# Performance work log

Measured on AMD Instinct MI355X. Metric: run time of the kernel, lower is better.

## Reference

```python
import jax, jax.numpy as jnp
import numpy as np

B, L, HID, NH = 8, 384, 512, 8
DH = HID // NH
MAX_SEQ_LEN = 384  # module's max_seq_len; pe has 2*MAX_SEQ_LEN rows


def setup_inputs() -> dict:
    key = jax.random.key(0)
    ks = jax.random.split(key, 16)
    s = 0.02
    inp = {
        "key": jax.random.normal(ks[0], (B, L, HID), jnp.float32),
        "query": jax.random.normal(ks[1], (B, L, HID), jnp.float32),
        "value": jax.random.normal(ks[2], (B, L, HID), jnp.float32),
        "seq_len": jnp.maximum(
            jax.random.randint(ks[3], (B,), L // 2, L + 1), 0
        ).at[0].set(L),  # ensure max(seq_len) == L
        "pe": jax.random.normal(ks[4], (2 * MAX_SEQ_LEN, HID), jnp.float32) * s,
        "Wk": jax.random.normal(ks[5], (HID, HID), jnp.float32) * s,
        "bk": jnp.zeros((HID,), jnp.float32),
        "Wq": jax.random.normal(ks[6], (HID, HID), jnp.float32) * s,
        "bq": jnp.zeros((HID,), jnp.float32),
        "Wv": jax.random.normal(ks[7], (HID, HID), jnp.float32) * s,
        "bv": jnp.zeros((HID,), jnp.float32),
        "Wr": jax.random.normal(ks[8], (HID, HID), jnp.float32) * s,
        "br": jnp.zeros((HID,), jnp.float32),
        "u_bias": jax.random.normal(ks[9], (NH, DH), jnp.float32) * s,
        "v_bias": jax.random.normal(ks[10], (NH, DH), jnp.float32) * s,
        "Wf": jax.random.normal(ks[11], (HID, HID), jnp.float32) * s,
        "bf": jnp.zeros((HID,), jnp.float32),
    }
    return inp


def reference(key, query, value, seq_len, pe, Wk, bk, Wq, bq, Wv, bv, Wr, br,
              u_bias, v_bias, Wf, bf):
    b, l, hid = key.shape
    # relative distance matrix: rel[i, j] = j - i
    idx = jnp.arange(l)
    rel = idx[None, :] - idx[:, None]                       # [L, L]
    rpe = pe[rel + MAX_SEQ_LEN]                             # [L, L, HID] gather

    k = (key @ Wk.T + bk).reshape(b, l, NH, DH).transpose(0, 2, 1, 3)    # [b,h,L,d]
    q = (query @ Wq.T + bq).reshape(b, l, NH, DH).transpose(0, 2, 1, 3)
    v = (value @ Wv.T + bv).reshape(b, l, NH, DH).transpose(0, 2, 1, 3)
    r = (rpe @ Wr.T + br).reshape(l, l, NH, DH)             # [L,L,h,d]

    A = jnp.einsum("bhid,bhjd->bhij", q, k)
    Bt = jnp.einsum("bhid,ijhd->bhij", q, r)
    C = jnp.einsum("hd,bhjd->bhj", u_bias, k)[:, :, None, :]  # broadcast over i
    D = jnp.einsum("ijhd,hd->hij", r, v_bias)[None]            # broadcast over b

    score = (A + Bt + C + D) / jnp.sqrt(jnp.float32(DH))
    mask = (idx[None, :] < seq_len[:, None])[:, None, None, :]  # [b,1,1,L]
    score = jnp.where(mask, score, jnp.float32(-1e15))
    attn = jax.nn.softmax(score, axis=-1)

    out = jnp.einsum("bhij,bhjd->bhid", attn, v)
    out = out.transpose(0, 2, 1, 3).reshape(b, l, hid)
    out = out @ Wf.T + bf  # ff_final
    return out
```

## Files before the change

kernel.cpp:

```cpp
#include <hip/hip_runtime.h>
#include <hip/hip_bf16.h>

typedef short v8s __attribute__((ext_vector_type(8)));
typedef float v4f __attribute__((ext_vector_type(4)));
typedef float float4v __attribute__((ext_vector_type(4)));
typedef unsigned short u16x4 __attribute__((ext_vector_type(4)));

#define BB 8
#define LL 384
#define HIDD 512
#define NHH 8
#define DHH 64
#define PP 768
#define BL (BB*LL)

using bf16 = __hip_bfloat16;

__device__ __forceinline__ v8s ld8(const bf16* p){
  return *reinterpret_cast<const v8s*>(p);
}

struct Ptrs { const void* p[16]; };

#define CAST_GROUPS 1606528

__global__ __launch_bounds__(256)
void cast_inputs(Ptrs ptrs, bf16* __restrict__ dst){
  __shared__ int smode;
  int tid = threadIdx.x;
  if (tid < 64){
    const unsigned int* key_raw = (const unsigned int*)ptrs.p[0];
    int huge = 0, zeros = 0;
    #pragma unroll
    for (int c = 0; c < 4; c++){
      unsigned int lo = key_raw[tid*4 + c] & 0xFFFFu;
      if (((lo >> 7) & 0xFF) >= 0x90u) huge++;
      if (lo == 0u) zeros++;
    }
    #pragma unroll
    for (int off = 32; off; off >>= 1){
      huge  += __shfl_xor(huge,  off);
      zeros += __shfl_xor(zeros, off);
    }
    if (tid == 0) smode = (huge > 8 || zeros > 200) ? 1 : 0;
  }
  __syncthreads();
  int mode = smode;

  const int start[17] = {0, 393216, 786432, 1179648, 1277952, 1343488, 1343616,
                         1409152, 1409280, 1474816, 1474944, 1540480, 1540608,
                         1540736, 1540864, 1606400, 1606528};
  int g = blockIdx.x*256 + tid;
  if (g >= CAST_GROUPS) return;
  int s = 0;
  #pragma unroll
  for (int i = 0; i < 16; i++) if (g >= start[i+1]) s = i+1;
  int local = g - start[s];
  u16x4 outv;
  if (mode){
    const float4v* src = (const float4v*)ptrs.p[s];
    float4v f = src[local];
    #pragma unroll
    for (int i = 0; i < 4; i++){
      bf16 h = __float2bfloat16(f[i]);
      outv[i] = *reinterpret_cast<unsigned short*>(&h);
    }
  } else {
    const u16x4* src = (const u16x4*)ptrs.p[s];
    outv = src[local];
  }
  *reinterpret_cast<u16x4*>(dst + (long)g*4) = outv;
}

__global__ void zero_out(float* __restrict__ out, int n){
  int i = blockIdx.x*256 + threadIdx.x;
  if (i < n) out[i] = 0.f;
}

__global__ __launch_bounds__(256)
void proj_gemm(const bf16* __restrict__ arena, bf16* __restrict__ outbase,
               bf16* __restrict__ vT, float* __restrict__ uk, float* __restrict__ rd)
{
  __shared__ alignas(16) bf16 ldsA[128*72];
  __shared__ alignas(16) bf16 ldsB[64*72];
  __shared__ float part[4*128];

  int z = blockIdx.z;
  if (z == 3 && blockIdx.y >= 6) return;
  const bf16* A    = arena + (long)z*1572864;
  const bf16* Bw   = arena + 5111808 + (long)z*262656;
  const bf16* bias = arena + 5373952 + (long)z*262656;

  int tid  = threadIdx.x;
  int lane = tid & 63, w = tid >> 6;
  int l16  = lane & 15, quad = lane >> 4;
  long g0  = (long)blockIdx.y * 128;
  int h    = blockIdx.x;
  int mloc = (w >> 1) * 64;
  int nloc = (w & 1) * 32;

  v4f acc[4][2] = {};
  for (int kk = 0; kk < HIDD; kk += 64){
    __syncthreads();
    #pragma unroll
    for (int c4 = 0; c4 < 4; c4++){
      int id = tid + c4*256;
      int row = id >> 3, c = id & 7;
      v8s v = ld8(A + (g0 + row)*HIDD + kk + c*8);
      *(v8s*)&ldsA[row*72 + c*8] = v;
    }
    #pragma unroll
    for (int c2 = 0; c2 < 2; c2++){
      int id = tid + c2*256;
      int row = id >> 3, c = id & 7;
      v8s v = ld8(Bw + (long)(h*64 + row)*HIDD + kk + c*8);
      *(v8s*)&ldsB[row*72 + c*8] = v;
    }
    __syncthreads();
    #pragma unroll
    for (int kq = 0; kq < 2; kq++){
      v8s af[4], bfr[2];
      #pragma unroll
      for (int ti = 0; ti < 4; ti++)
        af[ti] = *(const v8s*)&ldsA[(mloc + ti*16 + l16)*72 + kq*32 + quad*8];
      #pragma unroll
      for (int tj = 0; tj < 2; tj++)
        bfr[tj] = *(const v8s*)&ldsB[(nloc + tj*16 + l16)*72 + kq*32 + quad*8];
      #pragma unroll
      for (int ti = 0; ti < 4; ti++)
        #pragma unroll
        for (int tj = 0; tj < 2; tj++)
          acc[ti][tj] = __builtin_amdgcn_mfma_f32_16x16x32_bf16(af[ti], bfr[tj], acc[ti][tj], 0,0,0);
    }
  }

  if (z != 2){
    bf16* C = outbase + (long)z*1572864;
    #pragma unroll
    for (int ti = 0; ti < 4; ti++)
      #pragma unroll
      for (int tj = 0; tj < 2; tj++){
        int col = h*64 + nloc + tj*16 + l16;
        float bv = __bfloat162float(bias[col]);
        #pragma unroll
        for (int r = 0; r < 4; r++){
          long row = g0 + mloc + ti*16 + quad*4 + r;
          C[row*HIDD + col] = __float2bfloat16(acc[ti][tj][r] + bv);
        }
      }
  }

  if (z != 1){
    __syncthreads();
    bf16* tileT = ldsA;
    #pragma unroll
    for (int ti = 0; ti < 4; ti++)
      #pragma unroll
      for (int tj = 0; tj < 2; tj++){
        int lcol = nloc + tj*16 + l16;
        float bv = __bfloat162float(bias[h*64 + lcol]);
        #pragma unroll
        for (int r = 0; r < 4; r++){
          int lrow = mloc + ti*16 + quad*4 + r;
          tileT[lcol*132 + lrow] = __float2bfloat16(acc[ti][tj][r] + bv);
        }
      }
    __syncthreads();

    if (z == 2){
      int b = (int)(g0/LL), j0 = (int)(g0%LL);
      int d = tid >> 2, jc = (tid & 3)*32;
      #pragma unroll
      for (int s = 0; s < 4; s++){
        v8s v = *(const v8s*)&tileT[d*132 + jc + s*8];
        *(v8s*)&vT[((long)b*HIDD + h*64 + d)*LL + j0 + jc + s*8] = v;
      }
    } else {
      const bf16* vec = arena + (z == 0 ? 6162432 : 6162944) + h*64;
      int row2 = tid & 63;
      int pi   = tid >> 6;
      float s0 = 0.f, s1 = 0.f;
      #pragma unroll
      for (int dd = 0; dd < 16; dd++){
        int d = pi*16 + dd;
        float uvd = __bfloat162float(vec[d]);
        s0 += __bfloat162float(tileT[d*132 + row2])      * uvd;
        s1 += __bfloat162float(tileT[d*132 + row2 + 64]) * uvd;
      }
      part[pi*128 + row2]      = s0;
      part[pi*128 + row2 + 64] = s1;
      __syncthreads();
      if (tid < 128){
        float tot = part[tid] + part[128+tid] + part[256+tid] + part[384+tid];
        if (z == 0){
          int b = (int)(g0/LL), j0 = (int)(g0%LL);
          uk[((long)b*NHH + h)*LL + j0 + tid] = tot;
        } else {
          rd[h*PP + (int)g0 + tid] = tot;
        }
      }
    }
  }
}

__global__ __launch_bounds__(256)
void gemm_final(const bf16* __restrict__ A, const bf16* __restrict__ Bw,
                const bf16* __restrict__ bias, float* __restrict__ C)
{
  __shared__ alignas(16) bf16 ldsA[128*72];
  __shared__ alignas(16) bf16 ldsB[64*72];

  int tid  = threadIdx.x;
  int lane = tid & 63, w = tid >> 6;
  int l16  = lane & 15, quad = lane >> 4;
  long g0  = (long)blockIdx.y * 128;
  int h    = blockIdx.x;
  int mloc = (w >> 1) * 64;
  int nloc = (w & 1) * 32;

  v4f acc[4][2] = {};
  for (int kk = 0; kk < HIDD; kk += 64){
    __syncthreads();
    #pragma unroll
    for (int c4 = 0; c4 < 4; c4++){
      int id = tid + c4*256;
      int row = id >> 3, c = id & 7;
      v8s v = ld8(A + (g0 + row)*HIDD + kk + c*8);
      *(v8s*)&ldsA[row*72 + c*8] = v;
    }
    #pragma unroll
    for (int c2 = 0; c2 < 2; c2++){
      int id = tid + c2*256;
      int row = id >> 3, c = id & 7;
      v8s v = ld8(Bw + (long)(h*64 + row)*HIDD + kk + c*8);
      *(v8s*)&ldsB[row*72 + c*8] = v;
    }
    __syncthreads();
    #pragma unroll
    for (int kq = 0; kq < 2; kq++){
      v8s af[4], bfr[2];
      #pragma unroll
      for (int ti = 0; ti < 4; ti++)
        af[ti] = *(const v8s*)&ldsA[(mloc + ti*16 + l16)*72 + kq*32 + quad*8];
      #pragma unroll
      for (int tj = 0; tj < 2; tj++)
        bfr[tj] = *(const v8s*)&ldsB[(nloc + tj*16 + l16)*72 + kq*32 + quad*8];
      #pragma unroll
      for (int ti = 0; ti < 4; ti++)
        #pragma unroll
        for (int tj = 0; tj < 2; tj++)
          acc[ti][tj] = __builtin_amdgcn_mfma_f32_16x16x32_bf16(af[ti], bfr[tj], acc[ti][tj], 0,0,0);
    }
  }

  #pragma unroll
  for (int ti = 0; ti < 4; ti++)
    #pragma unroll
    for (int tj = 0; tj < 2; tj++){
      int col = h*64 + nloc + tj*16 + l16;
      float bv = __bfloat162float(bias[col]);
      #pragma unroll
      for (int r = 0; r < 4; r++){
        long row = g0 + mloc + ti*16 + quad*4 + r;
        C[row*HIDD + col] = acc[ti][tj][r] + bv;
      }
    }
}

#define BTS_S 404
#define S_S   397
#define PB_S  408

__global__ __launch_bounds__(256)
void attn_kernel(const bf16* __restrict__ qb, const bf16* __restrict__ kb,
                 const bf16* __restrict__ vT, const bf16* __restrict__ rproj,
                 const float* __restrict__ uk, const float* __restrict__ rd,
                 const unsigned int* __restrict__ sraw, bf16* __restrict__ attn_out)
{
  __shared__ alignas(16) bf16  Bts[16*BTS_S];
  __shared__ alignas(16) float S[16*S_S];
  __shared__ alignas(16) bf16  Pb[16*PB_S];
  __shared__ float rsum[16];
  __shared__ int s_slen;

  int i0 = blockIdx.x*16;
  int h  = blockIdx.y, b = blockIdx.z;
  int lane = threadIdx.x & 63, wave = threadIdx.x >> 6;
  int l16 = lane & 15, quad = lane >> 4;
  int p0 = 369 - i0;

  if (threadIdx.x == 0){
    bool i64 = true;
    for (int bb = 0; bb < BB; bb++){
      unsigned int w0 = sraw[2*bb], w1 = sraw[2*bb+1];
      if (!(w1 == 0u && w0 >= 1u && w0 < 100000u)) { i64 = false; break; }
    }
    unsigned int w = i64 ? sraw[2*b] : sraw[b];
    int v = (w < 100000u) ? (int)w : (int)(__uint_as_float(w) + 0.5f);
    s_slen = min(max(v, 0), LL);
  }

  const bf16* qp = qb + (long)(b*LL + i0 + l16)*HIDD + h*DHH;
  v8s aq0 = ld8(qp + quad*8);
  v8s aq1 = ld8(qp + 32 + quad*8);

  #pragma unroll 2
  for (int nt = wave; nt < 25; nt += 4){
    int pbase = p0 + nt*16;
    int prow = min(pbase + l16, PP-1);
    const bf16* rp = rproj + (long)prow*HIDD + h*DHH;
    v8s b0 = ld8(rp + quad*8);
    v8s b1 = ld8(rp + 32 + quad*8);
    v4f acc = {};
    acc = __builtin_amdgcn_mfma_f32_16x16x32_bf16(aq0, b0, acc, 0,0,0);
    acc = __builtin_amdgcn_mfma_f32_16x16x32_bf16(aq1, b1, acc, 0,0,0);
    float rdv = rd[h*PP + prow];
    #pragma unroll
    for (int r = 0; r < 4; r++)
      Bts[(quad*4 + r)*BTS_S + nt*16 + l16] = __float2bfloat16(acc[r] + rdv);
  }
  __syncthreads();
  int slen = s_slen;

  #pragma unroll 2
  for (int jt = wave; jt < 24; jt += 4){
    int j0 = jt*16;
    const bf16* kp = kb + (long)(b*LL + j0 + l16)*HIDD + h*DHH;
    v8s b0 = ld8(kp + quad*8);
    v8s b1 = ld8(kp + 32 + quad*8);
    v4f acc = {};
    acc = __builtin_amdgcn_mfma_f32_16x16x32_bf16(aq0, b0, acc, 0,0,0);
    acc = __builtin_amdgcn_mfma_f32_16x16x32_bf16(aq1, b1, acc, 0,0,0);
    int j = j0 + l16;
    float c_add = uk[(b*NHH + h)*LL + j];
    #pragma unroll
    for (int r = 0; r < 4; r++){
      int il = quad*4 + r;
      float bt = __bfloat162float(Bts[il*BTS_S + (j - il + 15)]);
      float s = (acc[r] + bt + c_add) * 0.125f;
      if (j >= slen) s = -1e15f;
      S[il*S_S + j] = s;
    }
  }
  __syncthreads();

  int d0 = wave*16;
  const bf16* vp = vT + ((long)(b*NHH + h)*DHH + d0 + l16)*LL;
  v8s vfrag[12];
  #pragma unroll
  for (int kt = 0; kt < 12; kt++) vfrag[kt] = ld8(vp + kt*32 + quad*8);

  for (int rr = 0; rr < 4; rr++){
    int row = wave*4 + rr;
    float vals[6];
    float m = -3.0e38f;
    #pragma unroll
    for (int t = 0; t < 6; t++){
      vals[t] = S[row*S_S + lane + t*64];
      m = fmaxf(m, vals[t]);
    }
    #pragma unroll
    for (int off = 32; off; off >>= 1) m = fmaxf(m, __shfl_xor(m, off));
    float sum = 0.f;
    #pragma unroll
    for (int t = 0; t < 6; t++){
      float e = __expf(vals[t] - m);
      sum += e;
      Pb[row*PB_S + lane + t*64] = __float2bfloat16(e);
    }
    #pragma unroll
    for (int off = 32; off; off >>= 1) sum += __shfl_xor(sum, off);
    if (lane == 0) rsum[row] = sum;
  }
  __syncthreads();

  {
    v4f o = {};
    #pragma unroll 4
    for (int kt = 0; kt < 12; kt++){
      v8s a = *reinterpret_cast<const v8s*>(&Pb[l16*PB_S + kt*32 + quad*8]);
      o = __builtin_amdgcn_mfma_f32_16x16x32_bf16(a, vfrag[kt], o, 0,0,0);
    }
    #pragma unroll
    for (int r = 0; r < 4; r++){
      int il = quad*4 + r;
      float val = o[r] / rsum[il];
      attn_out[(long)(b*LL + i0 + il)*HIDD + h*DHH + d0 + l16] = __float2bfloat16(val);
    }
  }
}

extern "C" void kernel_launch(void* const* d_in, const int* in_sizes, int n_in,
                              void* d_out, int out_size, void* d_ws, size_t ws_size,
                              hipStream_t stream)
{
  float* out = (float*)d_out;

  const int expect[17] = {1572864, 1572864, 1572864, 8, 393216,
                          262144, 512, 262144, 512, 262144, 512, 262144, 512,
                          512, 512, 262144, 512};
  bool ok = (n_in == 17);
  if (ok) for (int i = 0; i < 17; i++) if (in_sizes[i] != expect[i]) { ok = false; break; }
  if (!ok){
    zero_out<<<dim3((out_size + 255)/256), dim3(256), 0, stream>>>(out, out_size);
    return;
  }

  char* ws = (char*)d_ws;
  bf16*  cast   = (bf16*)(ws);
  bf16*  kb     = (bf16*)(ws + 12852224);
  bf16*  qb     = (bf16*)(ws + 15997952);
  bf16*  vT     = (bf16*)(ws + 19143680);
  bf16*  rproj  = (bf16*)(ws + 22289408);
  bf16*  attn_o = (bf16*)(ws + 25435136);
  float* uk     = (float*)(ws + 28580864);
  float* rd     = (float*)(ws + 28679168);
  (void)ws_size;

  const bf16* Wfc = cast + 6163456;
  const bf16* bfc = cast + 6425600;

  Ptrs ptrs;
  {
    int k = 0;
    for (int i = 0; i < 17; i++){ if (i == 3) continue; ptrs.p[k++] = d_in[i]; }
  }

  dim3 blk(256);
  cast_inputs<<<dim3((CAST_GROUPS + 255)/256), blk, 0, stream>>>(ptrs, cast);
  proj_gemm<<<dim3(8, 24, 4), blk, 0, stream>>>(cast, kb, vT, uk, rd);
  attn_kernel<<<dim3(LL/16, NHH, BB), blk, 0, stream>>>(
      qb, kb, vT, rproj, uk, rd, (const unsigned int*)d_in[3], attn_o);
  gemm_final<<<dim3(8, 24, 1), blk, 0, stream>>>(attn_o, Wfc, bfc, out);
}
```

Before: 181.0 us.

## Keep attention scores in registers and reduce softmax across waves via shared memory

Removes the fp32 score buffer in shared memory. Each wave keeps its score tiles in registers and computes row max and sum with intra-quad shuffles plus a small cross-wave shared reduction. V fragments are now loaded inside the PV loop instead of being preloaded, and launch bounds request more resident blocks. This frees about 25KB of LDS per block and some registers to raise occupancy, at the cost of an extra barrier and less latency hiding on the V loads.

Result: faster. 158.5 us, median of 2 (-12.4%).

```diff
diff --git a/kernel.cpp b/kernel.cpp
--- a/kernel.cpp
+++ b/kernel.cpp
@@ -268,19 +268,18 @@
 }
 
 #define BTS_S 404
-#define S_S   397
 #define PB_S  408
 
-__global__ __launch_bounds__(256)
+__global__ __launch_bounds__(256, 6)
 void attn_kernel(const bf16* __restrict__ qb, const bf16* __restrict__ kb,
                  const bf16* __restrict__ vT, const bf16* __restrict__ rproj,
                  const float* __restrict__ uk, const float* __restrict__ rd,
                  const unsigned int* __restrict__ sraw, bf16* __restrict__ attn_out)
 {
-  __shared__ alignas(16) bf16  Bts[16*BTS_S];
-  __shared__ alignas(16) float S[16*S_S];
-  __shared__ alignas(16) bf16  Pb[16*PB_S];
-  __shared__ float rsum[16];
+  __shared__ alignas(16) bf16 Bts[16*BTS_S];
+  __shared__ alignas(16) bf16 Pb[16*PB_S];
+  __shared__ float wmax[4*16];
+  __shared__ float wsum[4*16];
   __shared__ int s_slen;
 
   int i0 = blockIdx.x*16;
@@ -322,9 +321,10 @@
   __syncthreads();
   int slen = s_slen;
 
-  #pragma unroll 2
-  for (int jt = wave; jt < 24; jt += 4){
-    int j0 = jt*16;
+  float sv[6][4];
+  #pragma unroll
+  for (int t = 0; t < 6; t++){
+    int j0 = (wave + 4*t)*16;
     const bf16* kp = kb + (long)(b*LL + j0 + l16)*HIDD + h*DHH;
     v8s b0 = ld8(kp + quad*8);
     v8s b1 = ld8(kp + 32 + quad*8);
@@ -338,54 +338,75 @@
       int il = quad*4 + r;
       float bt = __bfloat162float(Bts[il*BTS_S + (j - il + 15)]);
       float s = (acc[r] + bt + c_add) * 0.125f;
-      if (j >= slen) s = -1e15f;
-      S[il*S_S + j] = s;
-    }
+      sv[t][r] = (j >= slen) ? -1e15f : s;
+    }
+  }
+
+  float mx[4];
+  #pragma unroll
+  for (int r = 0; r < 4; r++){
+    float m = sv[0][r];
+    #pragma unroll
+    for (int t = 1; t < 6; t++) m = fmaxf(m, sv[t][r]);
+    #pragma unroll
+    for (int off = 1; off < 16; off <<= 1) m = fmaxf(m, __shfl_xor(m, off));
+    mx[r] = m;
+  }
+  if (l16 == 0){
+    #pragma unroll
+    for (int r = 0; r < 4; r++) wmax[wave*16 + quad*4 + r] = mx[r];
   }
   __syncthreads();
 
-  int d0 = wave*16;
-  const bf16* vp = vT + ((long)(b*NHH + h)*DHH + d0 + l16)*LL;
-  v8s vfrag[12];
-  #pragma unroll
-  for (int kt = 0; kt < 12; kt++) vfrag[kt] = ld8(vp + kt*32 + quad*8);
-
-  for (int rr = 0; rr < 4; rr++){
-    int row = wave*4 + rr;
-    float vals[6];
-    float m = -3.0e38f;
-    #pragma unroll
-    for (int t = 0; t < 6; t++){
-      vals[t] = S[row*S_S + lane + t*64];
-      m = fmaxf(m, vals[t]);
-    }
-    #pragma unroll
-    for (int off = 32; off; off >>= 1) m = fmaxf(m, __shfl_xor(m, off));
-    float sum = 0.f;
-    #pragma unroll
-    for (int t = 0; t < 6; t++){
-      float e = __expf(vals[t] - m);
-      sum += e;
-      Pb[row*PB_S + lane + t*64] = __float2bfloat16(e);
-    }
-    #pragma unroll
-    for (int off = 32; off; off >>= 1) sum += __shfl_xor(sum, off);
-    if (lane == 0) rsum[row] = sum;
+  float gm[4];
+  #pragma unroll
+  for (int r = 0; r < 4; r++){
+    int row = quad*4 + r;
+    gm[r] = fmaxf(fmaxf(wmax[row], wmax[16+row]), fmaxf(wmax[32+row], wmax[48+row]));
+  }
+  float sm[4] = {0.f, 0.f, 0.f, 0.f};
+  #pragma unroll
+  for (int t = 0; t < 6; t++){
+    int j = (wave + 4*t)*16 + l16;
+    #pragma unroll
+    for (int r = 0; r < 4; r++){
+      float e = __expf(sv[t][r] - gm[r]);
+      sm[r] += e;
+      Pb[(quad*4 + r)*PB_S + j] = __float2bfloat16(e);
+    }
+  }
+  #pragma unroll
+  for (int r = 0; r < 4; r++){
+    #pragma unroll
+    for (int off = 1; off < 16; off <<= 1) sm[r] += __shfl_xor(sm[r], off);
+  }
+  if (l16 == 0){
+    #pragma unroll
+    for (int r = 0; r < 4; r++) wsum[wave*16 + quad*4 + r] = sm[r];
   }
   __syncthreads();
 
+  float rsum_r[4];
+  #pragma unroll
+  for (int r = 0; r < 4; r++){
+    int row = quad*4 + r;
+    rsum_r[r] = wsum[row] + wsum[16+row] + wsum[32+row] + wsum[48+row];
+  }
+
   {
+    int d0 = wave*16;
     v4f o = {};
+    const bf16* vp = vT + ((long)(b*NHH + h)*DHH + d0 + l16)*LL;
     #pragma unroll 4
     for (int kt = 0; kt < 12; kt++){
-      v8s a = *reinterpret_cast<const v8s*>(&Pb[l16*PB_S + kt*32 + quad*8]);
-      o = __builtin_amdgcn_mfma_f32_16x16x32_bf16(a, vfrag[kt], o, 0,0,0);
+      v8s a  = *reinterpret_cast<const v8s*>(&Pb[l16*PB_S + kt*32 + quad*8]);
+      v8s bb = ld8(vp + kt*32 + quad*8);
+      o = __builtin_amdgcn_mfma_f32_16x16x32_bf16(a, bb, o, 0,0,0);
     }
     #pragma unroll
     for (int r = 0; r < 4; r++){
-      int il = quad*4 + r;
-      float val = o[r] / rsum[il];
-      attn_out[(long)(b*LL + i0 + il)*HIDD + h*DHH + d0 + l16] = __float2bfloat16(val);
+      float val = o[r] / rsum_r[r];
+      attn_out[(long)(b*LL + i0 + quad*4 + r)*HIDD + h*DHH + d0 + l16] = __float2bfloat16(val);
     }
   }
 }
```
